# Kernel tuning notes

Measured on AMD Instinct MI355X. Metric: run time of the kernel, lower is better.

Reference implementation:

```python
import jax, jax.numpy as jnp
import numpy as np

N, L, C, K = 8, 16384, 256, 64  # batch, points, d_color, anchor_num; d_struct = 4*K = 256


def setup_inputs() -> dict:
    key = jax.random.key(0)
    ks = jax.random.split(key, 12)
    d_in = C + 4 * K  # 512
    s1, s2, s3 = 1.0 / np.sqrt(d_in), 1.0 / np.sqrt(128), 1.0 / np.sqrt(256)
    return {
        'feat0': jax.random.normal(ks[0], (N, L, C), jnp.float32),
        'feat1': jax.random.normal(ks[1], (N, L, C), jnp.float32),
        'pts_3d0': jax.random.normal(ks[2], (N, L, 3), jnp.float32),
        'pts_3d1': jax.random.normal(ks[3], (N, L, 3), jnp.float32),
        'anchor_i': jax.random.randint(ks[4], (N, K), 0, L, jnp.int32),
        'anchor_j': jax.random.randint(ks[5], (N, K), 0, L, jnp.int32),
        'W1': jax.random.uniform(ks[6], (d_in, 128), jnp.float32, -s1, s1),
        'b1': jax.random.uniform(ks[7], (128,), jnp.float32, -s1, s1),
        'W2': jax.random.uniform(ks[8], (128, 256), jnp.float32, -s2, s2),
        'b2': jax.random.uniform(ks[9], (256,), jnp.float32, -s2, s2),
        'W3': jax.random.uniform(ks[10], (256, C), jnp.float32, -s3, s3),
        'b3': jax.random.uniform(ks[11], (C,), jnp.float32, -s3, s3),
    }


def _structured(pts, anchor_idx):
    # pts: [N,L,3], anchor_idx: [N,K] -> [N,L,4K]
    anchors = jnp.take_along_axis(pts, anchor_idx[:, :, None], axis=1)  # [N,K,3]
    diff = pts[:, :, None, :] - anchors[:, None, :, :]                  # [N,L,K,3]
    dist = jnp.sum(diff * diff, axis=-1, keepdims=True)                 # [N,L,K,1]
    f = jnp.concatenate([diff, dist], axis=-1)                          # [N,L,K,4]
    f = f / jnp.sum(jnp.abs(f), axis=-2, keepdims=True)                 # L1 norm over K
    f = jnp.swapaxes(f, -1, -2).reshape(pts.shape[0], pts.shape[1], -1)  # [N,L,4K]
    # original l1_norm is @torch.no_grad -> structured feature is detached
    return jax.lax.stop_gradient(f)


def _mlp(x, W1, b1, W2, b2, W3, b3):
    h = jax.nn.relu(x @ W1 + b1)
    h = jax.nn.relu(h @ W2 + b2)  # dropout is identity in eval
    return h @ W3 + b3


def reference(feat0, feat1, pts_3d0, pts_3d1, anchor_i, anchor_j,
              W1, b1, W2, b2, W3, b3):
    s0 = _structured(pts_3d0, anchor_i)
    s1 = _structured(pts_3d1, anchor_j)
    aug0 = _mlp(jnp.concatenate([feat0, s0], axis=-1), W1, b1, W2, b2, W3, b3)
    aug1 = _mlp(jnp.concatenate([feat1, s1], axis=-1), W1, b1, W2, b2, W3, b3)
    return aug0, aug1
```

## Files before the change

kernel.cpp:

```cpp
#include <hip/hip_runtime.h>

typedef __bf16 bf16x8 __attribute__((ext_vector_type(8)));
typedef float f32x4 __attribute__((ext_vector_type(4)));
typedef unsigned short u16x4 __attribute__((ext_vector_type(4)));

#define NBATCH 8
#define LPTS   16384
#define CDIM   256
#define KANC   64
#define DIN    512
#define H1DIM  128
#define H2DIM  256
#define TM     64

__device__ __forceinline__ unsigned short f2b(float f){
  __bf16 h = (__bf16)f;
  return __builtin_bit_cast(unsigned short, h);
}

#define LBAR() do{ \
  asm volatile("s_waitcnt lgkmcnt(0)" ::: "memory"); \
  __builtin_amdgcn_s_barrier(); \
  asm volatile("" ::: "memory"); \
} while(0)

__global__ __launch_bounds__(256) void prep_weights(
    const float* __restrict__ W1, const float* __restrict__ W2,
    const float* __restrict__ W3, unsigned short* __restrict__ wt){
  int id = blockIdx.x * 256 + threadIdx.x;
  if (id < 65536){
    int r = id >> 9, c = id & 511;
    wt[id] = f2b(W1[c * 128 + r]);
  } else if (id < 98304){
    int t = id - 65536; int r = t >> 7, c = t & 127;
    wt[id] = f2b(W2[c * 256 + r]);
  } else if (id < 163840){
    int t = id - 98304; int r = t >> 8, c = t & 255;
    wt[id] = f2b(W3[c * 256 + r]);
  }
}

__global__ __launch_bounds__(128) void prep_coef(
    const float* __restrict__ pts0, const float* __restrict__ pts1,
    const int* __restrict__ anc_i, const int* __restrict__ anc_j,
    const float* __restrict__ W1, float* __restrict__ coef){
  const int comb = blockIdx.x;
  const int strm = comb >> 3, n = comb & 7;
  const int col  = threadIdx.x;
  __shared__ float4 anc[64];
  const float* pts  = strm ? pts1 : pts0;
  const int*   anci = strm ? anc_j : anc_i;
  if (col < 64){
    int ai = anci[n * KANC + col];
    const float* ap = pts + ((size_t)n * LPTS + ai) * 3;
    anc[col] = make_float4(ap[0], ap[1], ap[2], 0.f);
  }
  __syncthreads();
  float SX=0,CX=0,SY=0,CY=0,SZ=0,CZ=0,SD=0,ADx=0,ADy=0,ADz=0,CD2=0;
  float SAx=0,SAy=0,SAz=0,SA2=0;
  for (int k = 0; k < KANC; ++k){
    float4 a = anc[k];
    float ak2 = a.x*a.x + a.y*a.y + a.z*a.z;
    float wx = W1[(256 + k) * 128 + col];
    float wy = W1[(320 + k) * 128 + col];
    float wz = W1[(384 + k) * 128 + col];
    float wd = W1[(448 + k) * 128 + col];
    SX += wx; CX += a.x * wx;
    SY += wy; CY += a.y * wy;
    SZ += wz; CZ += a.z * wz;
    SD += wd; ADx += a.x * wd; ADy += a.y * wd; ADz += a.z * wd;
    CD2 += ak2 * wd;
    SAx += a.x; SAy += a.y; SAz += a.z; SA2 += ak2;
  }
  float* cf = coef + (size_t)comb * 12 * 128;
  cf[ 0*128+col]=SX;  cf[ 1*128+col]=CX;  cf[ 2*128+col]=SY;  cf[ 3*128+col]=CY;
  cf[ 4*128+col]=SZ;  cf[ 5*128+col]=CZ;  cf[ 6*128+col]=SD;  cf[ 7*128+col]=ADx;
  cf[ 8*128+col]=ADy; cf[ 9*128+col]=ADz; cf[10*128+col]=CD2;
  if (col == 0) cf[11*128+0] = SAx;
  if (col == 1) cf[11*128+1] = SAy;
  if (col == 2) cf[11*128+2] = SAz;
  if (col == 3) cf[11*128+3] = SA2;
}

__global__ __launch_bounds__(512, 4) void fused(
    const float* __restrict__ feat0, const float* __restrict__ feat1,
    const float* __restrict__ pts0, const float* __restrict__ pts1,
    const int* __restrict__ anc_i, const int* __restrict__ anc_j,
    const float* __restrict__ b1, const float* __restrict__ b2,
    const float* __restrict__ b3, const unsigned short* __restrict__ wt,
    const float* __restrict__ coef, float* __restrict__ out)
{
  __shared__ unsigned short xs[TM * 256];
  __shared__ unsigned short h1s[TM * H1DIM];
  __shared__ float scal[TM][12];
  unsigned short* h2s = xs;

  const int tid  = threadIdx.x;
  const int wg   = blockIdx.x;
  const int strm = wg >> 11;
  const int n    = (wg >> 8) & 7;
  const int l0   = (wg & 255) * TM;

  const float* feat = strm ? feat1 : feat0;
  const float* pts  = strm ? pts1 : pts0;
  const int*   anci = strm ? anc_j : anc_i;
  const float* cf   = coef + (size_t)((strm << 3) | n) * 12 * 128;

  const int lane = tid & 63;
  const int w    = tid >> 6;
  const int lr   = lane & 15;
  const int lg   = lane >> 4;
  const int col1 = w * 16 + lr;
  const int col0 = w * 32;
  const unsigned short* wrow1 = wt + col1 * DIN;
  const unsigned short* w2t = wt + 65536;
  const unsigned short* w3t = wt + 98304;

  float ax, ay, az;
  {
    int ai = anci[n * KANC + lane];
    const float* ap = pts + ((size_t)n * LPTS + ai) * 3;
    ax = ap[0]; ay = ap[1]; az = ap[2];
  }
  const float* pp = pts + ((size_t)n * LPTS + l0 + (tid >> 3)) * 3;
  float px = pp[0], py = pp[1], pz = pp[2];
  float SAx = cf[11*128+0], SAy = cf[11*128+1], SAz = cf[11*128+2], SA2 = cf[11*128+3];
  float cc[11];
  #pragma unroll
  for (int j = 0; j < 11; ++j) cc[j] = cf[j * 128 + col1];
  float bias1 = b1[col1];
  bf16x8 g1b[4];
  #pragma unroll
  for (int kk = 0; kk < 4; ++kk) g1b[kk] = *(const bf16x8*)&wrow1[kk * 32 + lg * 8];
  bf16x8 g2b0 = *(const bf16x8*)&w2t[(col0      + lr) * H1DIM + lg * 8];
  bf16x8 g2b1 = *(const bf16x8*)&w2t[(col0 + 16 + lr) * H1DIM + lg * 8];
  bf16x8 g3b0 = *(const bf16x8*)&w3t[(col0      + lr) * H2DIM + lg * 8];
  bf16x8 g3b1 = *(const bf16x8*)&w3t[(col0 + 16 + lr) * H2DIM + lg * 8];

  {
    const float4* fb = (const float4*)(feat + ((size_t)n * LPTS + l0) * CDIM);
    #pragma unroll
    for (int it = 0; it < 8; ++it){
      int flat = it * 512 + tid;
      int r = flat >> 6, c4 = flat & 63;
      float4 v = fb[flat];
      int e = (r * 256 + c4 * 4) ^ ((r & 7) << 3);
      u16x4 pk = { f2b(v.x), f2b(v.y), f2b(v.z), f2b(v.w) };
      *(u16x4*)&xs[e] = pk;
    }
  }

  {
    const int l   = tid >> 3;
    const int sub = tid & 7;
    float s0 = 0.f, s1 = 0.f, s2 = 0.f;
    #pragma unroll
    for (int i = 0; i < 8; ++i){
      int src = sub * 8 + i;
      float akx = __shfl(ax, src, 64);
      float aky = __shfl(ay, src, 64);
      float akz = __shfl(az, src, 64);
      s0 += fabsf(px - akx); s1 += fabsf(py - aky); s2 += fabsf(pz - akz);
    }
    #pragma unroll
    for (int m = 1; m <= 4; m <<= 1){
      s0 += __shfl_xor(s0, m, 64);
      s1 += __shfl_xor(s1, m, 64);
      s2 += __shfl_xor(s2, m, 64);
    }
    float pp2 = px*px + py*py + pz*pz;
    float s3 = 64.f * pp2 - 2.f * (px*SAx + py*SAy + pz*SAz) + SA2;
    float i0 = 1.f/s0, i1 = 1.f/s1, i2 = 1.f/s2, i3 = 1.f/s3;
    float u;
    switch (sub){
      case 0: u = i0 * px;       break;
      case 1: u = -i0;           break;
      case 2: u = i1 * py;       break;
      case 3: u = -i1;           break;
      case 4: u = i2 * pz;       break;
      case 5: u = -i2;           break;
      case 6: u = i3 * pp2;      break;
      default: u = -2.f*i3*px;   break;
    }
    scal[l][sub] = u;
    if (sub < 3){
      float u2 = (sub == 0) ? -2.f*i3*py : (sub == 1) ? -2.f*i3*pz : i3;
      scal[l][8 + sub] = u2;
    }
  }
  LBAR();

  {
    f32x4 acc[4] = {};
    #pragma unroll
    for (int kk = 0; kk < 8; ++kk){
      int kb = kk * 32 + lg * 8;
      bf16x8 b = (kk < 4) ? g1b[kk] : *(const bf16x8*)&wrow1[kb];
      #pragma unroll
      for (int m = 0; m < 4; ++m){
        int row = m * 16 + lr;
        bf16x8 a = *(const bf16x8*)&xs[(row * 256 + kb) ^ ((row & 7) << 3)];
        acc[m] = __builtin_amdgcn_mfma_f32_16x16x32_bf16(a, b, acc[m], 0, 0, 0);
      }
    }
    #pragma unroll
    for (int m = 0; m < 4; ++m){
      #pragma unroll
      for (int r = 0; r < 4; ++r){
        int row = m * 16 + lg * 4 + r;
        f32x4 ua = *(const f32x4*)&scal[row][0];
        f32x4 ub = *(const f32x4*)&scal[row][4];
        f32x4 uc = *(const f32x4*)&scal[row][8];
        float s = acc[m][r] + bias1;
        s += ua[0]*cc[0] + ua[1]*cc[1] + ua[2]*cc[2] + ua[3]*cc[3];
        s += ub[0]*cc[4] + ub[1]*cc[5] + ub[2]*cc[6] + ub[3]*cc[7];
        s += uc[0]*cc[8] + uc[1]*cc[9] + uc[2]*cc[10];
        float v = fmaxf(s, 0.f);
        h1s[(row * H1DIM + col1) ^ ((row & 7) << 3)] = f2b(v);
      }
    }
  }
  LBAR();

  {
    f32x4 acc[4][2] = {};
    #pragma unroll
    for (int kk = 0; kk < 4; ++kk){
      int kb = kk * 32 + lg * 8;
      bf16x8 bf0 = (kk == 0) ? g2b0 : *(const bf16x8*)&w2t[(col0 + lr) * H1DIM + kb];
      bf16x8 bf1 = (kk == 0) ? g2b1 : *(const bf16x8*)&w2t[(col0 + 16 + lr) * H1DIM + kb];
      #pragma unroll
      for (int m = 0; m < 4; ++m){
        int row = m * 16 + lr;
        bf16x8 a = *(const bf16x8*)&h1s[(row * H1DIM + kb) ^ ((row & 7) << 3)];
        acc[m][0] = __builtin_amdgcn_mfma_f32_16x16x32_bf16(a, bf0, acc[m][0], 0, 0, 0);
        acc[m][1] = __builtin_amdgcn_mfma_f32_16x16x32_bf16(a, bf1, acc[m][1], 0, 0, 0);
      }
    }
    #pragma unroll
    for (int nt = 0; nt < 2; ++nt){
      int col = col0 + nt * 16 + lr;
      float bias = b2[col];
      #pragma unroll
      for (int m = 0; m < 4; ++m){
        #pragma unroll
        for (int r = 0; r < 4; ++r){
          int row = m * 16 + lg * 4 + r;
          float v = fmaxf(acc[m][nt][r] + bias, 0.f);
          h2s[(row * H2DIM + col) ^ ((row & 7) << 3)] = f2b(v);
        }
      }
    }
  }
  LBAR();

  {
    f32x4 acc[4][2] = {};
    #pragma unroll 4
    for (int kk = 0; kk < 8; ++kk){
      int kb = kk * 32 + lg * 8;
      bf16x8 bf0 = (kk == 0) ? g3b0 : *(const bf16x8*)&w3t[(col0 + lr) * H2DIM + kb];
      bf16x8 bf1 = (kk == 0) ? g3b1 : *(const bf16x8*)&w3t[(col0 + 16 + lr) * H2DIM + kb];
      #pragma unroll
      for (int m = 0; m < 4; ++m){
        int row = m * 16 + lr;
        bf16x8 a = *(const bf16x8*)&h2s[(row * H2DIM + kb) ^ ((row & 7) << 3)];
        acc[m][0] = __builtin_amdgcn_mfma_f32_16x16x32_bf16(a, bf0, acc[m][0], 0, 0, 0);
        acc[m][1] = __builtin_amdgcn_mfma_f32_16x16x32_bf16(a, bf1, acc[m][1], 0, 0, 0);
      }
    }
    float* ob = out + (((size_t)strm * NBATCH + n) * LPTS + l0) * CDIM;
    #pragma unroll
    for (int nt = 0; nt < 2; ++nt){
      int col = col0 + nt * 16 + lr;
      float bias = b3[col];
      #pragma unroll
      for (int m = 0; m < 4; ++m){
        #pragma unroll
        for (int r = 0; r < 4; ++r){
          int row = m * 16 + lg * 4 + r;
          ob[(size_t)row * CDIM + col] = acc[m][nt][r] + bias;
        }
      }
    }
  }
}

extern "C" void kernel_launch(void* const* d_in, const int* in_sizes, int n_in,
                              void* d_out, int out_size, void* d_ws, size_t ws_size,
                              hipStream_t stream){
  const float* feat0 = (const float*)d_in[0];
  const float* feat1 = (const float*)d_in[1];
  const float* pts0  = (const float*)d_in[2];
  const float* pts1  = (const float*)d_in[3];
  const int*   anci  = (const int*)d_in[4];
  const int*   ancj  = (const int*)d_in[5];
  const float* W1    = (const float*)d_in[6];
  const float* b1    = (const float*)d_in[7];
  const float* W2    = (const float*)d_in[8];
  const float* b2    = (const float*)d_in[9];
  const float* W3    = (const float*)d_in[10];
  const float* b3    = (const float*)d_in[11];
  unsigned short* wt = (unsigned short*)d_ws;
  float* coef = (float*)((char*)d_ws + 163840 * sizeof(unsigned short));
  float* out = (float*)d_out;

  prep_weights<<<640, 256, 0, stream>>>(W1, W2, W3, wt);
  prep_coef<<<16, 128, 0, stream>>>(pts0, pts1, anci, ancj, W1, coef);
  fused<<<4096, 512, 0, stream>>>(feat0, feat1, pts0, pts1, anci, ancj,
                                  b1, b2, b3, wt, coef, out);
}
```

Baseline: 211.6 us.

## Process two 64-row tiles per workgroup and prefetch second tile's features

Each workgroup now handles 128 points as two 64-row halves, and the grid is halved. The second half's feature rows are loaded into registers while the first half's MLP runs, so global load latency overlaps with MFMA work. It also amortises the per-workgroup anchor, coefficient and bias setup. In exchange, register pressure rises (16 float4 feature buffers held live, with launch bounds of 512 threads and 4 blocks), the weight-register preloads are dropped, and an extra barrier is added per half.

```diff
diff --git a/kernel.cpp b/kernel.cpp
--- a/kernel.cpp
+++ b/kernel.cpp
@@ -97,9 +97,9 @@
 
   const int tid  = threadIdx.x;
   const int wg   = blockIdx.x;
-  const int strm = wg >> 11;
-  const int n    = (wg >> 8) & 7;
-  const int l0   = (wg & 255) * TM;
+  const int strm = wg >> 10;
+  const int n    = (wg >> 7) & 7;
+  const int l0   = (wg & 127) * 128;
 
   const float* feat = strm ? feat1 : feat0;
   const float* pts  = strm ? pts1 : pts0;
@@ -122,167 +122,186 @@
     const float* ap = pts + ((size_t)n * LPTS + ai) * 3;
     ax = ap[0]; ay = ap[1]; az = ap[2];
   }
-  const float* pp = pts + ((size_t)n * LPTS + l0 + (tid >> 3)) * 3;
-  float px = pp[0], py = pp[1], pz = pp[2];
+  const float* ppb = pts + ((size_t)n * LPTS + l0 + (tid >> 3)) * 3;
+  float px0 = ppb[0],       py0 = ppb[1],       pz0 = ppb[2];
+  float px1 = ppb[64*3],    py1 = ppb[64*3+1],  pz1 = ppb[64*3+2];
   float SAx = cf[11*128+0], SAy = cf[11*128+1], SAz = cf[11*128+2], SA2 = cf[11*128+3];
   float cc[11];
   #pragma unroll
   for (int j = 0; j < 11; ++j) cc[j] = cf[j * 128 + col1];
   float bias1 = b1[col1];
-  bf16x8 g1b[4];
+  float bias2a = b2[col0 + lr], bias2b = b2[col0 + 16 + lr];
+  float bias3a = b3[col0 + lr], bias3b = b3[col0 + 16 + lr];
+
+  const float4* fb = (const float4*)(feat + ((size_t)n * LPTS + l0) * CDIM);
+  float4 fvA[8];
   #pragma unroll
-  for (int kk = 0; kk < 4; ++kk) g1b[kk] = *(const bf16x8*)&wrow1[kk * 32 + lg * 8];
-  bf16x8 g2b0 = *(const bf16x8*)&w2t[(col0      + lr) * H1DIM + lg * 8];
-  bf16x8 g2b1 = *(const bf16x8*)&w2t[(col0 + 16 + lr) * H1DIM + lg * 8];
-  bf16x8 g3b0 = *(const bf16x8*)&w3t[(col0      + lr) * H2DIM + lg * 8];
-  bf16x8 g3b1 = *(const bf16x8*)&w3t[(col0 + 16 + lr) * H2DIM + lg * 8];
-
+  for (int it = 0; it < 8; ++it) fvA[it] = fb[it * 512 + tid];
+  float4 fvB[8];
+
+  float u0a, u0b, u1a, u1b;
   {
-    const float4* fb = (const float4*)(feat + ((size_t)n * LPTS + l0) * CDIM);
-    #pragma unroll
-    for (int it = 0; it < 8; ++it){
-      int flat = it * 512 + tid;
-      int r = flat >> 6, c4 = flat & 63;
-      float4 v = fb[flat];
-      int e = (r * 256 + c4 * 4) ^ ((r & 7) << 3);
-      u16x4 pk = { f2b(v.x), f2b(v.y), f2b(v.z), f2b(v.w) };
-      *(u16x4*)&xs[e] = pk;
-    }
-  }
-
-  {
-    const int l   = tid >> 3;
     const int sub = tid & 7;
-    float s0 = 0.f, s1 = 0.f, s2 = 0.f;
+    float s00=0.f,s01=0.f,s02=0.f, s10=0.f,s11=0.f,s12=0.f;
     #pragma unroll
     for (int i = 0; i < 8; ++i){
       int src = sub * 8 + i;
       float akx = __shfl(ax, src, 64);
       float aky = __shfl(ay, src, 64);
       float akz = __shfl(az, src, 64);
-      s0 += fabsf(px - akx); s1 += fabsf(py - aky); s2 += fabsf(pz - akz);
+      s00 += fabsf(px0 - akx); s01 += fabsf(py0 - aky); s02 += fabsf(pz0 - akz);
+      s10 += fabsf(px1 - akx); s11 += fabsf(py1 - aky); s12 += fabsf(pz1 - akz);
     }
     #pragma unroll
     for (int m = 1; m <= 4; m <<= 1){
-      s0 += __shfl_xor(s0, m, 64);
-      s1 += __shfl_xor(s1, m, 64);
-      s2 += __shfl_xor(s2, m, 64);
-    }
-    float pp2 = px*px + py*py + pz*pz;
-    float s3 = 64.f * pp2 - 2.f * (px*SAx + py*SAy + pz*SAz) + SA2;
-    float i0 = 1.f/s0, i1 = 1.f/s1, i2 = 1.f/s2, i3 = 1.f/s3;
-    float u;
-    switch (sub){
-      case 0: u = i0 * px;       break;
-      case 1: u = -i0;           break;
-      case 2: u = i1 * py;       break;
-      case 3: u = -i1;           break;
-      case 4: u = i2 * pz;       break;
-      case 5: u = -i2;           break;
-      case 6: u = i3 * pp2;      break;
-      default: u = -2.f*i3*px;   break;
-    }
-    scal[l][sub] = u;
-    if (sub < 3){
+      s00 += __shfl_xor(s00, m, 64); s01 += __shfl_xor(s01, m, 64);
+      s02 += __shfl_xor(s02, m, 64);
+      s10 += __shfl_xor(s10, m, 64); s11 += __shfl_xor(s11, m, 64);
+      s12 += __shfl_xor(s12, m, 64);
+    }
+    #pragma unroll
+    for (int half = 0; half < 2; ++half){
+      float px = half ? px1 : px0, py = half ? py1 : py0, pz = half ? pz1 : pz0;
+      float s0 = half ? s10 : s00, s1 = half ? s11 : s01, s2 = half ? s12 : s02;
+      float pp2 = px*px + py*py + pz*pz;
+      float s3 = 64.f * pp2 - 2.f * (px*SAx + py*SAy + pz*SAz) + SA2;
+      float i0 = 1.f/s0, i1 = 1.f/s1, i2 = 1.f/s2, i3 = 1.f/s3;
+      float u;
+      switch (sub){
+        case 0: u = i0 * px;       break;
+        case 1: u = -i0;           break;
+        case 2: u = i1 * py;       break;
+        case 3: u = -i1;           break;
+        case 4: u = i2 * pz;       break;
+        case 5: u = -i2;           break;
+        case 6: u = i3 * pp2;      break;
+        default: u = -2.f*i3*px;   break;
+      }
       float u2 = (sub == 0) ? -2.f*i3*py : (sub == 1) ? -2.f*i3*pz : i3;
-      scal[l][8 + sub] = u2;
-    }
-  }
-  LBAR();
-
-  {
-    f32x4 acc[4] = {};
-    #pragma unroll
-    for (int kk = 0; kk < 8; ++kk){
-      int kb = kk * 32 + lg * 8;
-      bf16x8 b = (kk < 4) ? g1b[kk] : *(const bf16x8*)&wrow1[kb];
-      #pragma unroll
-      for (int m = 0; m < 4; ++m){
-        int row = m * 16 + lr;
-        bf16x8 a = *(const bf16x8*)&xs[(row * 256 + kb) ^ ((row & 7) << 3)];
-        acc[m] = __builtin_amdgcn_mfma_f32_16x16x32_bf16(a, b, acc[m], 0, 0, 0);
-      }
-    }
-    #pragma unroll
-    for (int m = 0; m < 4; ++m){
-      #pragma unroll
-      for (int r = 0; r < 4; ++r){
-        int row = m * 16 + lg * 4 + r;
-        f32x4 ua = *(const f32x4*)&scal[row][0];
-        f32x4 ub = *(const f32x4*)&scal[row][4];
-        f32x4 uc = *(const f32x4*)&scal[row][8];
-        float s = acc[m][r] + bias1;
-        s += ua[0]*cc[0] + ua[1]*cc[1] + ua[2]*cc[2] + ua[3]*cc[3];
-        s += ub[0]*cc[4] + ub[1]*cc[5] + ub[2]*cc[6] + ub[3]*cc[7];
-        s += uc[0]*cc[8] + uc[1]*cc[9] + uc[2]*cc[10];
-        float v = fmaxf(s, 0.f);
-        h1s[(row * H1DIM + col1) ^ ((row & 7) << 3)] = f2b(v);
-      }
-    }
-  }
-  LBAR();
-
-  {
-    f32x4 acc[4][2] = {};
-    #pragma unroll
-    for (int kk = 0; kk < 4; ++kk){
-      int kb = kk * 32 + lg * 8;
-      bf16x8 bf0 = (kk == 0) ? g2b0 : *(const bf16x8*)&w2t[(col0 + lr) * H1DIM + kb];
-      bf16x8 bf1 = (kk == 0) ? g2b1 : *(const bf16x8*)&w2t[(col0 + 16 + lr) * H1DIM + kb];
-      #pragma unroll
-      for (int m = 0; m < 4; ++m){
-        int row = m * 16 + lr;
-        bf16x8 a = *(const bf16x8*)&h1s[(row * H1DIM + kb) ^ ((row & 7) << 3)];
-        acc[m][0] = __builtin_amdgcn_mfma_f32_16x16x32_bf16(a, bf0, acc[m][0], 0, 0, 0);
-        acc[m][1] = __builtin_amdgcn_mfma_f32_16x16x32_bf16(a, bf1, acc[m][1], 0, 0, 0);
-      }
-    }
-    #pragma unroll
-    for (int nt = 0; nt < 2; ++nt){
-      int col = col0 + nt * 16 + lr;
-      float bias = b2[col];
+      if (half){ u1a = u; u1b = u2; } else { u0a = u; u0b = u2; }
+    }
+  }
+
+  #pragma unroll
+  for (int half = 0; half < 2; ++half){
+    {
+      #pragma unroll
+      for (int it = 0; it < 8; ++it){
+        int flat = it * 512 + tid;
+        int r = flat >> 6, c4 = flat & 63;
+        float4 v = half ? fvB[it] : fvA[it];
+        int e = (r * 256 + c4 * 4) ^ ((r & 7) << 3);
+        u16x4 pk = { f2b(v.x), f2b(v.y), f2b(v.z), f2b(v.w) };
+        *(u16x4*)&xs[e] = pk;
+      }
+    }
+    {
+      const int l = tid >> 3, sub = tid & 7;
+      scal[l][sub] = half ? u1a : u0a;
+      if (sub < 3) scal[l][8 + sub] = half ? u1b : u0b;
+    }
+    if (half == 0){
+      const float4* fb1 = fb + 4096;
+      #pragma unroll
+      for (int it = 0; it < 8; ++it) fvB[it] = fb1[it * 512 + tid];
+    }
+    LBAR();
+
+    {
+      f32x4 acc[4] = {};
+      #pragma unroll
+      for (int kk = 0; kk < 8; ++kk){
+        int kb = kk * 32 + lg * 8;
+        bf16x8 b = *(const bf16x8*)&wrow1[kb];
+        #pragma unroll
+        for (int m = 0; m < 4; ++m){
+          int row = m * 16 + lr;
+          bf16x8 a = *(const bf16x8*)&xs[(row * 256 + kb) ^ ((row & 7) << 3)];
+          acc[m] = __builtin_amdgcn_mfma_f32_16x16x32_bf16(a, b, acc[m], 0, 0, 0);
+        }
+      }
       #pragma unroll
       for (int m = 0; m < 4; ++m){
         #pragma unroll
         for (int r = 0; r < 4; ++r){
           int row = m * 16 + lg * 4 + r;
-          float v = fmaxf(acc[m][nt][r] + bias, 0.f);
-          h2s[(row * H2DIM + col) ^ ((row & 7) << 3)] = f2b(v);
-        }
-      }
-    }
-  }
-  LBAR();
-
-  {
-    f32x4 acc[4][2] = {};
-    #pragma unroll 4
-    for (int kk = 0; kk < 8; ++kk){
-      int kb = kk * 32 + lg * 8;
-      bf16x8 bf0 = (kk == 0) ? g3b0 : *(const bf16x8*)&w3t[(col0 + lr) * H2DIM + kb];
-      bf16x8 bf1 = (kk == 0) ? g3b1 : *(const bf16x8*)&w3t[(col0 + 16 + lr) * H2DIM + kb];
-      #pragma unroll
-      for (int m = 0; m < 4; ++m){
-        int row = m * 16 + lr;
-        bf16x8 a = *(const bf16x8*)&h2s[(row * H2DIM + kb) ^ ((row & 7) << 3)];
-        acc[m][0] = __builtin_amdgcn_mfma_f32_16x16x32_bf16(a, bf0, acc[m][0], 0, 0, 0);
-        acc[m][1] = __builtin_amdgcn_mfma_f32_16x16x32_bf16(a, bf1, acc[m][1], 0, 0, 0);
-      }
-    }
-    float* ob = out + (((size_t)strm * NBATCH + n) * LPTS + l0) * CDIM;
-    #pragma unroll
-    for (int nt = 0; nt < 2; ++nt){
-      int col = col0 + nt * 16 + lr;
-      float bias = b3[col];
-      #pragma unroll
-      for (int m = 0; m < 4; ++m){
-        #pragma unroll
-        for (int r = 0; r < 4; ++r){
-          int row = m * 16 + lg * 4 + r;
-          ob[(size_t)row * CDIM + col] = acc[m][nt][r] + bias;
-        }
-      }
-    }
+          f32x4 ua = *(const f32x4*)&scal[row][0];
+          f32x4 ub = *(const f32x4*)&scal[row][4];
+          f32x4 uc = *(const f32x4*)&scal[row][8];
+          float s = acc[m][r] + bias1;
+          s += ua[0]*cc[0] + ua[1]*cc[1] + ua[2]*cc[2] + ua[3]*cc[3];
+          s += ub[0]*cc[4] + ub[1]*cc[5] + ub[2]*cc[6] + ub[3]*cc[7];
+          s += uc[0]*cc[8] + uc[1]*cc[9] + uc[2]*cc[10];
+          float v = fmaxf(s, 0.f);
+          h1s[(row * H1DIM + col1) ^ ((row & 7) << 3)] = f2b(v);
+        }
+      }
+    }
+    LBAR();
+
+    {
+      f32x4 acc[4][2] = {};
+      #pragma unroll
+      for (int kk = 0; kk < 4; ++kk){
+        int kb = kk * 32 + lg * 8;
+        bf16x8 bf0 = *(const bf16x8*)&w2t[(col0 + lr) * H1DIM + kb];
+        bf16x8 bf1 = *(const bf16x8*)&w2t[(col0 + 16 + lr) * H1DIM + kb];
+        #pragma unroll
+        for (int m = 0; m < 4; ++m){
+          int row = m * 16 + lr;
+          bf16x8 a = *(const bf16x8*)&h1s[(row * H1DIM + kb) ^ ((row & 7) << 3)];
+          acc[m][0] = __builtin_amdgcn_mfma_f32_16x16x32_bf16(a, bf0, acc[m][0], 0, 0, 0);
+          acc[m][1] = __builtin_amdgcn_mfma_f32_16x16x32_bf16(a, bf1, acc[m][1], 0, 0, 0);
+        }
+      }
+      #pragma unroll
+      for (int nt = 0; nt < 2; ++nt){
+        float bias = nt ? bias2b : bias2a;
+        int col = col0 + nt * 16 + lr;
+        #pragma unroll
+        for (int m = 0; m < 4; ++m){
+          #pragma unroll
+          for (int r = 0; r < 4; ++r){
+            int row = m * 16 + lg * 4 + r;
+            float v = fmaxf(acc[m][nt][r] + bias, 0.f);
+            h2s[(row * H2DIM + col) ^ ((row & 7) << 3)] = f2b(v);
+          }
+        }
+      }
+    }
+    LBAR();
+
+    {
+      f32x4 acc[4][2] = {};
+      #pragma unroll 4
+      for (int kk = 0; kk < 8; ++kk){
+        int kb = kk * 32 + lg * 8;
+        bf16x8 bf0 = *(const bf16x8*)&w3t[(col0 + lr) * H2DIM + kb];
+        bf16x8 bf1 = *(const bf16x8*)&w3t[(col0 + 16 + lr) * H2DIM + kb];
+        #pragma unroll
+        for (int m = 0; m < 4; ++m){
+          int row = m * 16 + lr;
+          bf16x8 a = *(const bf16x8*)&h2s[(row * H2DIM + kb) ^ ((row & 7) << 3)];
+          acc[m][0] = __builtin_amdgcn_mfma_f32_16x16x32_bf16(a, bf0, acc[m][0], 0, 0, 0);
+          acc[m][1] = __builtin_amdgcn_mfma_f32_16x16x32_bf16(a, bf1, acc[m][1], 0, 0, 0);
+        }
+      }
+      float* ob = out + (((size_t)strm * NBATCH + n) * LPTS + l0 + half * 64) * CDIM;
+      #pragma unroll
+      for (int nt = 0; nt < 2; ++nt){
+        float bias = nt ? bias3b : bias3a;
+        int col = col0 + nt * 16 + lr;
+        #pragma unroll
+        for (int m = 0; m < 4; ++m){
+          #pragma unroll
+          for (int r = 0; r < 4; ++r){
+            int row = m * 16 + lg * 4 + r;
+            ob[(size_t)row * CDIM + col] = acc[m][nt][r] + bias;
+          }
+        }
+      }
+    }
+    LBAR();
   }
 }
 
@@ -307,6 +326,6 @@
 
   prep_weights<<<640, 256, 0, stream>>>(W1, W2, W3, wt);
   prep_coef<<<16, 128, 0, stream>>>(pts0, pts1, anci, ancj, W1, coef);
-  fused<<<4096, 512, 0, stream>>>(feat0, feat1, pts0, pts1, anci, ancj,
+  fused<<<2048, 512, 0, stream>>>(feat0, feat1, pts0, pts1, anci, ancj,
                                   b1, b2, b3, wt, coef, out);
 }
```

Result: slower. 553.7 us (+161.6%).
